# Kernel optimization log

Hardware: AMD Instinct MI355X
Metric: run time of the kernel (lower is better)

## Reference

```python
import jax, jax.numpy as jnp
import numpy as np

DIM, H, HD = 1024, 16, 64
B, S = 2, 2048
LAMBDA_INIT = 0.8


def _mha(x, wq, bq, wk, bk, wv, bv, wo, bo):
    # x: [B,S,DIM]; wq/wk/wv: [DIM,H,HD]; wo: [H,HD,DIM]
    q = jnp.einsum('btd,dhk->bthk', x, wq) + bq
    k = jnp.einsum('bsd,dhk->bshk', x, wk) + bk
    v = jnp.einsum('bsd,dhk->bshk', x, wv) + bv
    scores = jnp.einsum('bthk,bshk->bhts', q, k) / jnp.sqrt(jnp.asarray(HD, x.dtype))
    attn = jax.nn.softmax(scores, axis=-1)
    out = jnp.einsum('bhts,bshk->bthk', attn, v)
    return jnp.einsum('bthk,hkd->btd', out, wo) + bo


def _get_lambda(lambda_param, layer_idx):
    layer_factor = jnp.clip(jnp.asarray(layer_idx, jnp.float32) * 0.3, 0.0, 5.0)
    offset = 0.6 * jnp.exp(-layer_factor)
    lam = jax.nn.sigmoid(lambda_param) * (1.0 - offset) + 0.2
    return jnp.clip(lam, 0.1, 0.9)


def setup_inputs() -> dict:
    key = jax.random.key(0)
    ks = jax.random.split(key, 10)
    sc_in = 1.0 / np.sqrt(DIM)   # fan-in-ish scale for projections
    sc_out = 1.0 / np.sqrt(H * HD)
    d = {
        'x': jax.random.normal(ks[0], (B, S, DIM), jnp.float32),
        'proj_w': jax.random.normal(ks[1], (DIM, DIM), jnp.float32) * sc_in,
        'proj_b': jnp.zeros((DIM,), jnp.float32),
        'lambda_param': jnp.full((1,), np.log(LAMBDA_INIT) - np.log(1.0 - LAMBDA_INIT), jnp.float32),
        'layer_idx': 0,
    }
    for i, kk in zip((1, 2), (ks[2:6], ks[6:10])):
        d[f'wq{i}'] = jax.random.normal(kk[0], (DIM, H, HD), jnp.float32) * sc_in
        d[f'wk{i}'] = jax.random.normal(kk[1], (DIM, H, HD), jnp.float32) * sc_in
        d[f'wv{i}'] = jax.random.normal(kk[2], (DIM, H, HD), jnp.float32) * sc_in
        d[f'wo{i}'] = jax.random.normal(kk[3], (H, HD, DIM), jnp.float32) * sc_out
        d[f'bq{i}'] = jnp.zeros((H, HD), jnp.float32)
        d[f'bk{i}'] = jnp.zeros((H, HD), jnp.float32)
        d[f'bv{i}'] = jnp.zeros((H, HD), jnp.float32)
        d[f'bo{i}'] = jnp.zeros((DIM,), jnp.float32)
    return d


def reference(x, wq1, bq1, wk1, bk1, wv1, bv1, wo1, bo1,
              wq2, bq2, wk2, bk2, wv2, bv2, wo2, bo2,
              proj_w, proj_b, lambda_param, layer_idx):
    out1 = _mha(x, wq1, bq1, wk1, bk1, wv1, bv1, wo1, bo1)
    out2 = _mha(x, wq2, bq2, wk2, bk2, wv2, bv2, wo2, bo2)
    lam = _get_lambda(lambda_param, layer_idx)  # shape (1,)
    y = (1.0 - lam) * out1 + lam * out2
    return jnp.einsum('btd,de->bte', y, proj_w) + proj_b
```

## Files before the change

### kernel.cpp

```cpp
#include <hip/hip_runtime.h>

#define DEVI __device__ __forceinline__

typedef unsigned short u16;
typedef unsigned int u32;
typedef __bf16 bf16x8 __attribute__((ext_vector_type(8)));
typedef float f32x4 __attribute__((ext_vector_type(4)));
typedef float f32x16 __attribute__((ext_vector_type(16)));
typedef int i32x2v __attribute__((ext_vector_type(2)));

#define SCALE_Q 0.1803368801f

typedef const __attribute__((address_space(1))) void cas1_void;
typedef __attribute__((address_space(3))) void as3_void;

DEVI void lds_dma16(const void* g, void* l) {
  __builtin_amdgcn_global_load_lds((cas1_void*)g, (as3_void*)l, 16, 0, 0);
}

DEVI u16 f2bf(float f) {
  union { float f; u32 u; } v; v.f = f;
  u32 r = v.u + 0x7FFFu + ((v.u >> 16) & 1u);
  return (u16)(r >> 16);
}

DEVI float exp2n(float x) {
#if __has_builtin(__builtin_amdgcn_exp2f)
  return __builtin_amdgcn_exp2f(x);
#else
  return __expf(x * 0.6931471805599453f);
#endif
}

DEVI u32 pk2(float lo, float hi2) {
  union { __bf16 h[2]; u32 u; } p;
  p.h[0] = (__bf16)lo; p.h[1] = (__bf16)hi2;
  return p.u;
}

DEVI void plswap2(u32 a, u32 b, u32& x, u32& y) {
#if __has_builtin(__builtin_amdgcn_permlane32_swap)
  i32x2v r = __builtin_amdgcn_permlane32_swap((int)a, (int)b, false, false);
  x = (u32)r[0]; y = (u32)r[1];
#else
  u32 ta = __shfl_xor(a, 32), tb = __shfl_xor(b, 32);
  const int hi_ = (int)((threadIdx.x & 63) >> 5);
  x = hi_ ? tb : a;
  y = hi_ ? b : ta;
#endif
}

DEVI float lambda_dev(const float* lamp, const int* lidx) {
  float lf = (float)(*lidx) * 0.3f;
  lf = fminf(fmaxf(lf, 0.0f), 5.0f);
  float offset = 0.6f * expf(-lf);
  float s = 1.0f / (1.0f + expf(-lamp[0]));
  float lam = s * (1.0f - offset) + 0.2f;
  return fminf(fmaxf(lam, 0.1f), 0.9f);
}

__global__ __launch_bounds__(256) void k_cvt(const float* __restrict__ x, u16* __restrict__ o) {
  int i = (blockIdx.x * 256 + threadIdx.x) * 8;
  float4 a = *(const float4*)(x + i);
  float4 b = *(const float4*)(x + i + 4);
  union { u16 s[8]; uint4 v; } r;
  r.s[0] = f2bf(a.x); r.s[1] = f2bf(a.y); r.s[2] = f2bf(a.z); r.s[3] = f2bf(a.w);
  r.s[4] = f2bf(b.x); r.s[5] = f2bf(b.y); r.s[6] = f2bf(b.z); r.s[7] = f2bf(b.w);
  *(uint4*)(o + i) = r.v;
}

struct TransArgs {
  const float* src[9];
  u16* dst[9];
  int dld[9];
  int dcol[9];
  int smode[9];
};

__global__ __launch_bounds__(256) void k_transpose(TransArgs ta, const float* lamp, const int* lidx) {
  __shared__ float tile[32][33];
  int z = blockIdx.z;
  int tx = threadIdx.x & 31, ty = threadIdx.x >> 5;
  int bx = blockIdx.x * 32, by = blockIdx.y * 32;
  const float* s = ta.src[z];
#pragma unroll
  for (int i = 0; i < 4; ++i)
    tile[ty + i * 8][tx] = s[(size_t)(by + ty + i * 8) * 1024 + bx + tx];
  __syncthreads();
  float sc = 1.0f;
  int m = ta.smode[z];
  if (m == 1) sc = SCALE_Q;
  else if (m >= 2) {
    float lam = lambda_dev(lamp, lidx);
    sc = (m == 2) ? (1.0f - lam) : lam;
  }
  u16* d = ta.dst[z];
  size_t ld = (size_t)ta.dld[z];
#pragma unroll
  for (int i = 0; i < 4; ++i) {
    int dr = bx + ty + i * 8;
    d[(size_t)dr * ld + ta.dcol[z] + by + tx] = f2bf(sc * tile[tx][ty + i * 8]);
  }
}

struct GemmArgs {
  const u16* A;
  const u16* Bt[6];
  const float* bias0[6];
  float bscale[6];
  u16* dstu[6];
  const float* bias1;
  float* dstf;
  const float* lamp;
  const int* lidx;
  int K;
  int mode;
};

__global__ __launch_bounds__(256) void k_gemm(GemmArgs ga) {
  __shared__ __align__(16) u16 smem[32768];
  char* smc = (char*)smem;
  const int t = threadIdx.x;
  const int lane = t & 63;
  const int l15 = lane & 15, hi = lane >> 4;
  const int w = t >> 6, wm = w >> 1, wn = w & 1;
  const int m0 = blockIdx.y * 128, n0 = blockIdx.x * 128;
  const int z = (ga.mode == 0) ? (int)blockIdx.z : 0;
  const u16* A = ga.A;
  const u16* Bt = ga.Bt[z];
  const int K = ga.K;

  const char* gA[4];
  const char* gB[4];
  u32 lof[4];
#pragma unroll
  for (int ii = 0; ii < 4; ++ii) {
    int fl = ii * 256 + t;
    int row = fl >> 3;
    int cb = ((fl & 7) * 16) ^ ((row & 7) << 4);
    gA[ii] = (const char*)(A + (size_t)(m0 + row) * K) + cb;
    gB[ii] = (const char*)(Bt + (size_t)(n0 + row) * K) + cb;
    lof[ii] = (u32)(ii * 256 + (t & ~63)) * 16;
  }

  u32 aoff[4], boff[4];
#pragma unroll
  for (int i = 0; i < 4; ++i) {
    int rA = wm * 64 + i * 16 + l15;
    aoff[i] = (u32)rA * 128 + (u32)((hi * 16) ^ ((rA & 7) << 4));
    int rB = wn * 64 + i * 16 + l15;
    boff[i] = 16384u + (u32)rB * 128 + (u32)((hi * 16) ^ ((rB & 7) << 4));
  }

  const f32x4 fz = {0.f, 0.f, 0.f, 0.f};
  f32x4 acc[4][4];
#pragma unroll
  for (int i = 0; i < 4; ++i)
#pragma unroll
    for (int j = 0; j < 4; ++j) acc[i][j] = fz;

  const int NT = K >> 6;
#pragma unroll
  for (int ii = 0; ii < 4; ++ii) {
    lds_dma16(gA[ii], smc + lof[ii]);
    lds_dma16(gB[ii], smc + 16384 + lof[ii]);
  }
  __syncthreads();
  int cur = 0;
  for (int kt = 0; kt < NT; ++kt) {
    if (kt + 1 < NT) {
      const u32 nb = (u32)(cur ^ 1) * 32768u;
      size_t soff = (size_t)(kt + 1) * 128;
#pragma unroll
      for (int ii = 0; ii < 4; ++ii) {
        lds_dma16(gA[ii] + soff, smc + nb + lof[ii]);
        lds_dma16(gB[ii] + soff, smc + nb + 16384 + lof[ii]);
      }
    }
    const u32 bb = (u32)cur * 32768u;
#pragma unroll
    for (int kh = 0; kh < 2; ++kh) {
      const u32 kx = (u32)kh << 6;
      bf16x8 af[4], bfr[4];
#pragma unroll
      for (int i = 0; i < 4; ++i) af[i] = *(const bf16x8*)(smc + bb + (aoff[i] ^ kx));
#pragma unroll
      for (int j = 0; j < 4; ++j) bfr[j] = *(const bf16x8*)(smc + bb + (boff[j] ^ kx));
#pragma unroll
      for (int i = 0; i < 4; ++i)
#pragma unroll
        for (int j = 0; j < 4; ++j)
          acc[i][j] = __builtin_amdgcn_mfma_f32_16x16x32_bf16(af[i], bfr[j], acc[i][j], 0, 0, 0);
    }
    __syncthreads();
    cur ^= 1;
  }

  const int mode = ga.mode;
  float lam = 0.f;
  if (mode == 1) lam = lambda_dev(ga.lamp, ga.lidx);
  const float* b0 = ga.bias0[z];
  const float bsc = ga.bscale[z];
  const int kind = z % 3;
  u16* du = ga.dstu[z];

#pragma unroll
  for (int i = 0; i < 4; ++i) {
#pragma unroll
    for (int j = 0; j < 4; ++j) {
#pragma unroll
      for (int jj = 0; jj < 4; ++jj) {
        int m = m0 + wm * 64 + i * 16 + hi * 4 + jj;
        int n = n0 + wn * 64 + j * 16 + l15;
        float v = acc[i][j][jj];
        if (mode == 0) {
          v += b0[n] * bsc;
          int b = m >> 11, s = m & 2047, h = n >> 6, hd = n & 63;
          size_t addr;
          if (kind == 0) {
            addr = ((size_t)(b * 16 + h) * 2048 + s) * 64 + hd;
          } else if (kind == 1) {
            int gf = ((s >> 5) * 8 + (hd >> 4) * 2 + ((hd >> 3) & 1)) * 32 + (s & 31);
            addr = ((size_t)(b * 16 + h) * 16384 + gf) * 8 + (hd & 7);
          } else {
            int gf = ((((s >> 6) * 4 + ((s >> 4) & 3)) * 2 + ((s >> 3) & 1)) * 2 + (hd >> 5)) * 32 + (hd & 31);
            addr = ((size_t)(b * 16 + h) * 16384 + gf) * 8 + (s & 7);
          }
          du[addr] = f2bf(v);
        } else if (mode == 1) {
          v += (1.0f - lam) * b0[n] + lam * ga.bias1[n];
          du[(size_t)m * 1024 + n] = f2bf(v);
        } else {
          v += b0[n];
          ga.dstf[(size_t)m * 1024 + n] = v;
        }
      }
    }
  }
}

__global__ __launch_bounds__(256, 2) void k_attn3(const u16* __restrict__ Qg_, const u16* __restrict__ Kg_,
                                                  const u16* __restrict__ Vg_, u16* __restrict__ AO) {
  const int t = threadIdx.x, lane = t & 63, w = t >> 6;
  const int l31 = lane & 31, hi = lane >> 5;
  const int bid = blockIdx.x;
  const int xcd = bid & 7, slot = bid >> 3;
  const int qt = slot & 15;
  const int bhbr = xcd * 8 + (slot >> 4);
  const int br = bhbr >> 5, bh = bhbr & 31;
  const size_t base = ((size_t)br * 32 + bh) * 131072;
  const u16* Qg = Qg_ + base;
  const u16* Kt = Kg_ + base + (size_t)(hi * 256 + l31 * 8);
  const u16* Vt = Vg_ + base + (size_t)(hi * 512 + l31 * 8);
  const int q0 = qt * 128 + w * 32;

  bf16x8 qf[4];
  {
    const u16* qp = Qg + (size_t)(q0 + l31) * 64 + hi * 8;
#pragma unroll
    for (int ks = 0; ks < 4; ++ks) qf[ks] = *(const bf16x8*)(qp + ks * 16);
  }

  f32x16 accO[2];
#pragma unroll
  for (int b = 0; b < 2; ++b)
#pragma unroll
    for (int r = 0; r < 16; ++r) accO[b][r] = 0.f;
  float l_r = 0.f;

  bf16x8 kf[2][4], vf[2][4];
#pragma unroll
  for (int kvs = 0; kvs < 2; ++kvs)
#pragma unroll
    for (int ks = 0; ks < 4; ++ks)
      kf[kvs][ks] = *(const bf16x8*)(Kt + kvs * 2048 + ks * 512);
#pragma unroll
  for (int hs = 0; hs < 2; ++hs)
#pragma unroll
    for (int ks = 0; ks < 4; ++ks)
      vf[hs][ks] = *(const bf16x8*)(Vt + ks * 1024 + hs * 256);

  for (int kvt = 0; kvt < 32; ++kvt) {
    f32x16 st[2];
#pragma unroll
    for (int kvs = 0; kvs < 2; ++kvs)
#pragma unroll
      for (int r = 0; r < 16; ++r) st[kvs][r] = 0.f;
#pragma unroll
    for (int ks = 0; ks < 4; ++ks) {
      st[0] = __builtin_amdgcn_mfma_f32_32x32x16_bf16(kf[0][ks], qf[ks], st[0], 0, 0, 0);
      st[1] = __builtin_amdgcn_mfma_f32_32x32x16_bf16(kf[1][ks], qf[ks], st[1], 0, 0, 0);
    }
    if (kvt < 31) {
      const u16* kp = Kt + (size_t)(kvt + 1) * 4096;
#pragma unroll
      for (int kvs = 0; kvs < 2; ++kvs)
#pragma unroll
        for (int ks = 0; ks < 4; ++ks)
          kf[kvs][ks] = *(const bf16x8*)(kp + kvs * 2048 + ks * 512);
    }

    float sm0 = 0.f, sm1 = 0.f, sm2 = 0.f, sm3 = 0.f;
#pragma unroll
    for (int kvs = 0; kvs < 2; ++kvs)
#pragma unroll
      for (int r = 0; r < 16; r += 4) {
        float p0 = exp2n(st[kvs][r + 0]); st[kvs][r + 0] = p0; sm0 += p0;
        float p1 = exp2n(st[kvs][r + 1]); st[kvs][r + 1] = p1; sm1 += p1;
        float p2 = exp2n(st[kvs][r + 2]); st[kvs][r + 2] = p2; sm2 += p2;
        float p3 = exp2n(st[kvs][r + 3]); st[kvs][r + 3] = p3; sm3 += p3;
      }
    float sum = (sm0 + sm1) + (sm2 + sm3);
    sum += __shfl_xor(sum, 32);
    l_r += sum;

    bf16x8 pa[4];
#pragma unroll
    for (int kvs = 0; kvs < 2; ++kvs)
#pragma unroll
      for (int half = 0; half < 2; ++half) {
        const int rb = half * 8;
        u32 a0 = pk2(st[kvs][rb + 0], st[kvs][rb + 1]);
        u32 a1 = pk2(st[kvs][rb + 2], st[kvs][rb + 3]);
        u32 b0 = pk2(st[kvs][rb + 4], st[kvs][rb + 5]);
        u32 b1 = pk2(st[kvs][rb + 6], st[kvs][rb + 7]);
        u32 w0, w1, w2, w3;
        plswap2(a0, b0, w0, w2);
        plswap2(a1, b1, w1, w3);
        union { u32 u[4]; bf16x8 v; } pk;
        pk.u[0] = w0;
        pk.u[1] = w1;
        pk.u[2] = w2;
        pk.u[3] = w3;
        pa[kvs * 2 + half] = pk.v;
      }

#pragma unroll
    for (int ks = 0; ks < 4; ++ks) {
      accO[0] = __builtin_amdgcn_mfma_f32_32x32x16_bf16(pa[ks], vf[0][ks], accO[0], 0, 0, 0);
      accO[1] = __builtin_amdgcn_mfma_f32_32x32x16_bf16(pa[ks], vf[1][ks], accO[1], 0, 0, 0);
    }
    if (kvt < 31) {
      const u16* vp = Vt + (size_t)(kvt + 1) * 4096;
#pragma unroll
      for (int hs = 0; hs < 2; ++hs)
#pragma unroll
        for (int ks = 0; ks < 4; ++ks)
          vf[hs][ks] = *(const bf16x8*)(vp + ks * 1024 + hs * 256);
    }
  }

  const int b = bh >> 4, h = bh & 15;
  const float inv = 1.0f / l_r;
#pragma unroll
  for (int r = 0; r < 16; ++r) {
    const int qr = (r & 3) + 8 * (r >> 2) + 4 * hi;
    const float iv = __shfl(inv, qr);
    const size_t mrow = (size_t)(b * 2048 + q0 + qr);
#pragma unroll
    for (int hs = 0; hs < 2; ++hs) {
      const int col = br * 1024 + h * 64 + hs * 32 + l31;
      AO[mrow * 2048 + col] = f2bf(accO[hs][r] * iv);
    }
  }
}

extern "C" void kernel_launch(void* const* d_in, const int* in_sizes, int n_in,
                              void* d_out, int out_size, void* d_ws, size_t ws_size,
                              hipStream_t stream) {
  (void)in_sizes; (void)n_in; (void)out_size; (void)ws_size;
  const float* x      = (const float*)d_in[0];
  const float* proj_w = (const float*)d_in[1];
  const float* proj_b = (const float*)d_in[2];
  const float* lamp   = (const float*)d_in[3];
  const int*   lidx   = (const int*)d_in[4];
  const float* wq1 = (const float*)d_in[5];
  const float* wk1 = (const float*)d_in[6];
  const float* wv1 = (const float*)d_in[7];
  const float* wo1 = (const float*)d_in[8];
  const float* bq1 = (const float*)d_in[9];
  const float* bk1 = (const float*)d_in[10];
  const float* bv1 = (const float*)d_in[11];
  const float* bo1 = (const float*)d_in[12];
  const float* wq2 = (const float*)d_in[13];
  const float* wk2 = (const float*)d_in[14];
  const float* wv2 = (const float*)d_in[15];
  const float* wo2 = (const float*)d_in[16];
  const float* bq2 = (const float*)d_in[17];
  const float* bk2 = (const float*)d_in[18];
  const float* bv2 = (const float*)d_in[19];
  const float* bo2 = (const float*)d_in[20];

  char* ws = (char*)d_ws;
  const size_t MB = 1024 * 1024;
  u16* xb  = (u16*)(ws);
  u16* Wt  = (u16*)(ws + 8 * MB);
  u16* WOt = (u16*)(ws + 20 * MB);
  u16* PWt = (u16*)(ws + 24 * MB);
  u16* Qb  = (u16*)(ws + 26 * MB);
  u16* Kb  = (u16*)(ws + 42 * MB);
  u16* Vb  = (u16*)(ws + 58 * MB);
  u16* AOb = (u16*)(ws);
  u16* yb  = (u16*)(ws + 26 * MB);

  k_cvt<<<2048, 256, 0, stream>>>(x, xb);

  TransArgs ta;
  const float* srcs[9] = {wq1, wk1, wv1, wq2, wk2, wv2, wo1, wo2, proj_w};
  u16* dsts[9] = {Wt, Wt + 1048576, Wt + 2097152, Wt + 3145728, Wt + 4194304, Wt + 5242880,
                  WOt, WOt, PWt};
  int dld[9]   = {1024, 1024, 1024, 1024, 1024, 1024, 2048, 2048, 1024};
  int dcol[9]  = {0, 0, 0, 0, 0, 0, 0, 1024, 0};
  int smode[9] = {1, 0, 0, 1, 0, 0, 2, 3, 0};
  for (int i = 0; i < 9; ++i) {
    ta.src[i] = srcs[i]; ta.dst[i] = dsts[i]; ta.dld[i] = dld[i];
    ta.dcol[i] = dcol[i]; ta.smode[i] = smode[i];
  }
  k_transpose<<<dim3(32, 32, 9), 256, 0, stream>>>(ta, lamp, lidx);

  GemmArgs g0 = {};
  g0.A = xb; g0.K = 1024; g0.mode = 0;
  const float* qkvb[6] = {bq1, bk1, bv1, bq2, bk2, bv2};
  const size_t BRS = 4194304;
  u16* qkvd[6] = {Qb, Kb, Vb, Qb + BRS, Kb + BRS, Vb + BRS};
  float bsc[6] = {SCALE_Q, 1.f, 1.f, SCALE_Q, 1.f, 1.f};
  for (int i = 0; i < 6; ++i) {
    g0.Bt[i] = Wt + (size_t)i * 1048576;
    g0.bias0[i] = qkvb[i];
    g0.bscale[i] = bsc[i];
    g0.dstu[i] = qkvd[i];
  }
  k_gemm<<<dim3(8, 32, 6), 256, 0, stream>>>(g0);

  k_attn3<<<1024, 256, 0, stream>>>(Qb, Kb, Vb, AOb);

  GemmArgs g1 = {};
  g1.A = AOb; g1.K = 2048; g1.mode = 1;
  g1.Bt[0] = WOt; g1.bias0[0] = bo1; g1.bscale[0] = 1.f;
  g1.bias1 = bo2; g1.dstu[0] = yb; g1.lamp = lamp; g1.lidx = lidx;
  k_gemm<<<dim3(8, 32, 1), 256, 0, stream>>>(g1);

  GemmArgs g2 = {};
  g2.A = yb; g2.K = 1024; g2.mode = 2;
  g2.Bt[0] = PWt; g2.bias0[0] = proj_b; g2.bscale[0] = 1.f;
  g2.dstf = (float*)d_out;
  k_gemm<<<dim3(8, 32, 1), 256, 0, stream>>>(g2);
}
```

Measured before the change: 268.4 us.

## Fold output projection into combined Wo weights and remap QKV GEMM grid per XCD

Precomputes the product of the lambda-scaled output weights and proj_w as a weight-only GEMM, plus a fused bias vector. The attention output then needs a single K=2048 GEMM straight to fp32 output instead of two chained GEMMs. This drops the 4096x1024x1024 projection GEMM and the bf16 intermediate y, at the cost of a small weight-side GEMM and an extra rounding of the fused weights to bf16. The QKV GEMM also becomes a flat 1536-block launch with an XCD-aware mapping so blocks sharing weight columns land on the same XCD.

```diff
diff --git a/kernel.cpp b/kernel.cpp
--- a/kernel.cpp
+++ b/kernel.cpp
@@ -22,6 +22,10 @@
   union { float f; u32 u; } v; v.f = f;
   u32 r = v.u + 0x7FFFu + ((v.u >> 16) & 1u);
   return (u16)(r >> 16);
+}
+
+DEVI float bf2f(u16 v) {
+  union { u32 u; float f; } x; x.u = (u32)v << 16; return x.f;
 }
 
 DEVI float exp2n(float x) {
@@ -72,9 +76,8 @@
 struct TransArgs {
   const float* src[9];
   u16* dst[9];
-  int dld[9];
-  int dcol[9];
   int smode[9];
+  int tmode[9];
 };
 
 __global__ __launch_bounds__(256) void k_transpose(TransArgs ta, const float* lamp, const int* lidx) {
@@ -83,10 +86,6 @@
   int tx = threadIdx.x & 31, ty = threadIdx.x >> 5;
   int bx = blockIdx.x * 32, by = blockIdx.y * 32;
   const float* s = ta.src[z];
-#pragma unroll
-  for (int i = 0; i < 4; ++i)
-    tile[ty + i * 8][tx] = s[(size_t)(by + ty + i * 8) * 1024 + bx + tx];
-  __syncthreads();
   float sc = 1.0f;
   int m = ta.smode[z];
   if (m == 1) sc = SCALE_Q;
@@ -95,24 +94,57 @@
     sc = (m == 2) ? (1.0f - lam) : lam;
   }
   u16* d = ta.dst[z];
-  size_t ld = (size_t)ta.dld[z];
+  if (ta.tmode[z]) {
+#pragma unroll
+    for (int i = 0; i < 4; ++i)
+      tile[ty + i * 8][tx] = s[(size_t)(by + ty + i * 8) * 1024 + bx + tx];
+    __syncthreads();
+#pragma unroll
+    for (int i = 0; i < 4; ++i) {
+      int dr = bx + ty + i * 8;
+      d[(size_t)dr * 1024 + by + tx] = f2bf(sc * tile[tx][ty + i * 8]);
+    }
+  } else {
+#pragma unroll
+    for (int i = 0; i < 4; ++i) {
+      int r = by + ty + i * 8;
+      d[(size_t)r * 1024 + bx + tx] = f2bf(sc * s[(size_t)r * 1024 + bx + tx]);
+    }
+  }
+}
+
+__global__ __launch_bounds__(256) void k_bias2(const u16* __restrict__ PWt, const float* __restrict__ bo1,
+                                               const float* __restrict__ bo2, const float* __restrict__ pb,
+                                               const float* lamp, const int* lidx, float* __restrict__ b2) {
+  const float lam = lambda_dev(lamp, lidx);
+  const int lane = threadIdx.x & 63;
+  const int wv = blockIdx.x * 4 + (threadIdx.x >> 6);
 #pragma unroll
   for (int i = 0; i < 4; ++i) {
-    int dr = bx + ty + i * 8;
-    d[(size_t)dr * ld + ta.dcol[z] + by + tx] = f2bf(sc * tile[tx][ty + i * 8]);
+    const int e = wv * 4 + i;
+    const u16* row = PWt + (size_t)e * 1024 + lane * 16;
+    float acc = 0.f;
+#pragma unroll
+    for (int j = 0; j < 16; ++j) {
+      const int dd = lane * 16 + j;
+      const float bm = (1.0f - lam) * bo1[dd] + lam * bo2[dd];
+      acc += bf2f(row[j]) * bm;
+    }
+    acc += __shfl_xor(acc, 1);  acc += __shfl_xor(acc, 2);
+    acc += __shfl_xor(acc, 4);  acc += __shfl_xor(acc, 8);
+    acc += __shfl_xor(acc, 16); acc += __shfl_xor(acc, 32);
+    if (lane == 0) b2[e] = acc + pb[e];
   }
 }
 
 struct GemmArgs {
   const u16* A;
-  const u16* Bt[6];
+  const u16* Bt;
   const float* bias0[6];
   float bscale[6];
   u16* dstu[6];
-  const float* bias1;
+  u16* dst3;
   float* dstf;
-  const float* lamp;
-  const int* lidx;
   int K;
   int mode;
 };
@@ -124,10 +156,19 @@
   const int lane = t & 63;
   const int l15 = lane & 15, hi = lane >> 4;
   const int w = t >> 6, wm = w >> 1, wn = w & 1;
-  const int m0 = blockIdx.y * 128, n0 = blockIdx.x * 128;
-  const int z = (ga.mode == 0) ? (int)blockIdx.z : 0;
+  int m0, n0, z;
+  if (ga.mode == 0) {
+    const int bid = blockIdx.x;
+    const int xcd = bid & 7, local = bid >> 3;
+    const int nb = xcd * 6 + (local % 6);
+    m0 = (local / 6) * 128;
+    n0 = nb * 128;
+    z = n0 >> 10;
+  } else {
+    m0 = blockIdx.y * 128; n0 = blockIdx.x * 128; z = 0;
+  }
   const u16* A = ga.A;
-  const u16* Bt = ga.Bt[z];
+  const u16* Bt = ga.Bt;
   const int K = ga.K;
 
   const char* gA[4];
@@ -169,12 +210,12 @@
   int cur = 0;
   for (int kt = 0; kt < NT; ++kt) {
     if (kt + 1 < NT) {
-      const u32 nb = (u32)(cur ^ 1) * 32768u;
+      const u32 nb2 = (u32)(cur ^ 1) * 32768u;
       size_t soff = (size_t)(kt + 1) * 128;
 #pragma unroll
       for (int ii = 0; ii < 4; ++ii) {
-        lds_dma16(gA[ii] + soff, smc + nb + lof[ii]);
-        lds_dma16(gB[ii] + soff, smc + nb + 16384 + lof[ii]);
+        lds_dma16(gA[ii] + soff, smc + nb2 + lof[ii]);
+        lds_dma16(gB[ii] + soff, smc + nb2 + 16384 + lof[ii]);
       }
     }
     const u32 bb = (u32)cur * 32768u;
@@ -197,10 +238,8 @@
   }
 
   const int mode = ga.mode;
-  float lam = 0.f;
-  if (mode == 1) lam = lambda_dev(ga.lamp, ga.lidx);
-  const float* b0 = ga.bias0[z];
-  const float bsc = ga.bscale[z];
+  const float* b0 = ga.bias0[(mode == 0) ? z : 0];
+  const float bsc = (mode == 0) ? ga.bscale[z] : 1.0f;
   const int kind = z % 3;
   u16* du = ga.dstu[z];
 
@@ -214,8 +253,9 @@
         int n = n0 + wn * 64 + j * 16 + l15;
         float v = acc[i][j][jj];
         if (mode == 0) {
-          v += b0[n] * bsc;
-          int b = m >> 11, s = m & 2047, h = n >> 6, hd = n & 63;
+          int nz = n & 1023;
+          v += b0[nz] * bsc;
+          int b = m >> 11, s = m & 2047, h = nz >> 6, hd = nz & 63;
           size_t addr;
           if (kind == 0) {
             addr = ((size_t)(b * 16 + h) * 2048 + s) * 64 + hd;
@@ -227,9 +267,8 @@
             addr = ((size_t)(b * 16 + h) * 16384 + gf) * 8 + (s & 7);
           }
           du[addr] = f2bf(v);
-        } else if (mode == 1) {
-          v += (1.0f - lam) * b0[n] + lam * ga.bias1[n];
-          du[(size_t)m * 1024 + n] = f2bf(v);
+        } else if (mode == 3) {
+          ga.dst3[(size_t)m * 2048 + n] = f2bf(v);
         } else {
           v += b0[n];
           ga.dstf[(size_t)m * 1024 + n] = v;
@@ -328,10 +367,7 @@
         plswap2(a0, b0, w0, w2);
         plswap2(a1, b1, w1, w3);
         union { u32 u[4]; bf16x8 v; } pk;
-        pk.u[0] = w0;
-        pk.u[1] = w1;
-        pk.u[2] = w2;
-        pk.u[3] = w3;
+        pk.u[0] = w0; pk.u[1] = w1; pk.u[2] = w2; pk.u[3] = w3;
         pa[kvs * 2 + half] = pk.v;
       }
 
@@ -393,56 +429,55 @@
 
   char* ws = (char*)d_ws;
   const size_t MB = 1024 * 1024;
-  u16* xb  = (u16*)(ws);
-  u16* Wt  = (u16*)(ws + 8 * MB);
-  u16* WOt = (u16*)(ws + 20 * MB);
-  u16* PWt = (u16*)(ws + 24 * MB);
-  u16* Qb  = (u16*)(ws + 26 * MB);
-  u16* Kb  = (u16*)(ws + 42 * MB);
-  u16* Vb  = (u16*)(ws + 58 * MB);
-  u16* AOb = (u16*)(ws);
-  u16* yb  = (u16*)(ws + 26 * MB);
+  u16* xb   = (u16*)(ws);
+  u16* Wt   = (u16*)(ws + 8 * MB);
+  u16* WOt2 = (u16*)(ws + 20 * MB);
+  u16* PWt  = (u16*)(ws + 24 * MB);
+  u16* Qb   = (u16*)(ws + 26 * MB);
+  u16* Kb   = (u16*)(ws + 42 * MB);
+  u16* Vb   = (u16*)(ws + 58 * MB);
+  u16* Bt2  = (u16*)(ws + 74 * MB);
+  float* b2 = (float*)(ws + 78 * MB);
+  u16* AOb  = (u16*)(ws);
 
   k_cvt<<<2048, 256, 0, stream>>>(x, xb);
 
   TransArgs ta;
   const float* srcs[9] = {wq1, wk1, wv1, wq2, wk2, wv2, wo1, wo2, proj_w};
   u16* dsts[9] = {Wt, Wt + 1048576, Wt + 2097152, Wt + 3145728, Wt + 4194304, Wt + 5242880,
-                  WOt, WOt, PWt};
-  int dld[9]   = {1024, 1024, 1024, 1024, 1024, 1024, 2048, 2048, 1024};
-  int dcol[9]  = {0, 0, 0, 0, 0, 0, 0, 1024, 0};
+                  WOt2, WOt2 + 1048576, PWt};
   int smode[9] = {1, 0, 0, 1, 0, 0, 2, 3, 0};
+  int tmode[9] = {1, 1, 1, 1, 1, 1, 0, 0, 1};
   for (int i = 0; i < 9; ++i) {
-    ta.src[i] = srcs[i]; ta.dst[i] = dsts[i]; ta.dld[i] = dld[i];
-    ta.dcol[i] = dcol[i]; ta.smode[i] = smode[i];
+    ta.src[i] = srcs[i]; ta.dst[i] = dsts[i];
+    ta.smode[i] = smode[i]; ta.tmode[i] = tmode[i];
   }
   k_transpose<<<dim3(32, 32, 9), 256, 0, stream>>>(ta, lamp, lidx);
 
+  GemmArgs gw = {};
+  gw.A = PWt; gw.Bt = WOt2; gw.dst3 = Bt2; gw.K = 1024; gw.mode = 3;
+  k_gemm<<<dim3(16, 8), 256, 0, stream>>>(gw);
+
+  k_bias2<<<64, 256, 0, stream>>>(PWt, bo1, bo2, proj_b, lamp, lidx, b2);
+
   GemmArgs g0 = {};
-  g0.A = xb; g0.K = 1024; g0.mode = 0;
+  g0.A = xb; g0.Bt = Wt; g0.K = 1024; g0.mode = 0;
   const float* qkvb[6] = {bq1, bk1, bv1, bq2, bk2, bv2};
   const size_t BRS = 4194304;
   u16* qkvd[6] = {Qb, Kb, Vb, Qb + BRS, Kb + BRS, Vb + BRS};
   float bsc[6] = {SCALE_Q, 1.f, 1.f, SCALE_Q, 1.f, 1.f};
   for (int i = 0; i < 6; ++i) {
-    g0.Bt[i] = Wt + (size_t)i * 1048576;
     g0.bias0[i] = qkvb[i];
     g0.bscale[i] = bsc[i];
     g0.dstu[i] = qkvd[i];
   }
-  k_gemm<<<dim3(8, 32, 6), 256, 0, stream>>>(g0);
+  k_gemm<<<dim3(1536), 256, 0, stream>>>(g0);
 
   k_attn3<<<1024, 256, 0, stream>>>(Qb, Kb, Vb, AOb);
 
-  GemmArgs g1 = {};
-  g1.A = AOb; g1.K = 2048; g1.mode = 1;
-  g1.Bt[0] = WOt; g1.bias0[0] = bo1; g1.bscale[0] = 1.f;
-  g1.bias1 = bo2; g1.dstu[0] = yb; g1.lamp = lamp; g1.lidx = lidx;
-  k_gemm<<<dim3(8, 32, 1), 256, 0, stream>>>(g1);
-
   GemmArgs g2 = {};
-  g2.A = yb; g2.K = 1024; g2.mode = 2;
-  g2.Bt[0] = PWt; g2.bias0[0] = proj_b; g2.bscale[0] = 1.f;
+  g2.A = AOb; g2.Bt = Bt2; g2.K = 2048; g2.mode = 2;
+  g2.bias0[0] = b2;
   g2.dstf = (float*)d_out;
-  k_gemm<<<dim3(8, 32, 1), 256, 0, stream>>>(g2);
-}
+  k_gemm<<<dim3(8, 32), 256, 0, stream>>>(g2);
+}
```

After: 271.5 us. Within noise of the previous version (+1.1%).
